# Optimization experiments

Hardware: AMD Instinct MI355X
Metric: run time of the kernel (lower is better)

Reference implementation:

```python
import jax, jax.numpy as jnp
import numpy as np

KS = 5  # kernel_size
H, W = 2048, 2048


def setup_inputs() -> dict:
    key = jax.random.key(0)
    image = jax.random.normal(key, (H, W), dtype=jnp.float32)
    return {"image": image}


def reference(image):
    ks = KS
    r = ks // 2
    h, w = image.shape
    # reflect pad (matches torch F.pad mode='reflect')
    padded = jnp.pad(image, ((r, r), (r, r)), mode="reflect")  # (h+2r, w+2r)
    # gather the ks*ks shifted views -> (h, w, ks*ks); fixed small loop over offsets
    wins = jnp.stack(
        [padded[i : i + h, j : j + w] for i in range(ks) for j in range(ks)],
        axis=-1,
    )
    # torch .median returns the lower median = sorted index (n-1)//2 (exact median here since n=25 is odd)
    srt = jnp.sort(wins, axis=-1)
    return srt[..., (ks * ks - 1) // 2]
```

## Files before the change

### kernel.cpp

```cpp
#include <hip/hip_runtime.h>

constexpr int IMG_H = 2048;
constexpr int IMG_W = 2048;
constexpr int P = 8;

#define CE(a, b) {                                              \
    float _mn, _mx;                                             \
    asm("v_min_f32 %0, %1, %2" : "=v"(_mn) : "v"(a), "v"(b));   \
    asm("v_max_f32 %0, %1, %2" : "=v"(_mx) : "v"(a), "v"(b));   \
    a = _mn; b = _mx;                                           \
}

#define SORT3(a, b, c) {                                                      \
    float _n, _d, _x;                                                         \
    asm("v_min3_f32 %0, %1, %2, %3" : "=v"(_n) : "v"(a), "v"(b), "v"(c));     \
    asm("v_med3_f32 %0, %1, %2, %3" : "=v"(_d) : "v"(a), "v"(b), "v"(c));     \
    asm("v_max3_f32 %0, %1, %2, %3" : "=v"(_x) : "v"(a), "v"(b), "v"(c));     \
    a = _n; b = _d; c = _x;                                                   \
}

__device__ __forceinline__ void sw14(float& a0, float& a1, float& a2, float& a3, float& a4,
                                     float& a5, float& a6, float& a7, float& a8, float& a9,
                                     float& a10, float& a11, float& a12, float& a13) {
    SORT3(a0, a1, a2) SORT3(a3, a4, a5) SORT3(a6, a7, a8) SORT3(a9, a10, a11) CE(a12, a13)
    SORT3(a0, a3, a6) SORT3(a0, a9, a12)
    SORT3(a2, a5, a8) SORT3(a8, a11, a13)
}
__device__ __forceinline__ void sw13(float& a0, float& a1, float& a2, float& a3, float& a4,
                                     float& a5, float& a6, float& a7, float& a8, float& a9,
                                     float& a10, float& a11, float& a12) {
    SORT3(a0, a1, a2) SORT3(a3, a4, a5) SORT3(a6, a7, a8) SORT3(a9, a10, a11)
    SORT3(a0, a3, a6) SORT3(a0, a9, a12)
    SORT3(a2, a5, a8) SORT3(a8, a11, a12)
}
__device__ __forceinline__ void sw12(float& a0, float& a1, float& a2, float& a3, float& a4,
                                     float& a5, float& a6, float& a7, float& a8, float& a9,
                                     float& a10, float& a11) {
    SORT3(a0, a1, a2) SORT3(a3, a4, a5) SORT3(a6, a7, a8) SORT3(a9, a10, a11)
    SORT3(a0, a3, a6) CE(a0, a9)
    SORT3(a2, a5, a8) CE(a8, a11)
}
__device__ __forceinline__ void sw11(float& a0, float& a1, float& a2, float& a3, float& a4,
                                     float& a5, float& a6, float& a7, float& a8, float& a9,
                                     float& a10) {
    SORT3(a0, a1, a2) SORT3(a3, a4, a5) SORT3(a6, a7, a8) CE(a9, a10)
    SORT3(a0, a3, a6) CE(a0, a9)
    SORT3(a2, a5, a8) CE(a8, a10)
}
__device__ __forceinline__ void sw10(float& a0, float& a1, float& a2, float& a3, float& a4,
                                     float& a5, float& a6, float& a7, float& a8, float& a9) {
    SORT3(a0, a1, a2) SORT3(a3, a4, a5) SORT3(a6, a7, a8)
    SORT3(a0, a3, a6) CE(a0, a9)
    SORT3(a2, a5, a8) CE(a8, a9)
}
__device__ __forceinline__ void sw9(float& a0, float& a1, float& a2, float& a3, float& a4,
                                    float& a5, float& a6, float& a7, float& a8) {
    SORT3(a0, a1, a2) SORT3(a3, a4, a5) SORT3(a6, a7, a8)
    SORT3(a0, a3, a6)
    SORT3(a2, a5, a8)
}
__device__ __forceinline__ void sw8(float& a0, float& a1, float& a2, float& a3, float& a4,
                                    float& a5, float& a6, float& a7) {
    SORT3(a0, a1, a2) SORT3(a3, a4, a5) CE(a6, a7)
    SORT3(a0, a3, a6)
    SORT3(a2, a5, a7)
}
__device__ __forceinline__ void sw7(float& a0, float& a1, float& a2, float& a3, float& a4,
                                    float& a5, float& a6) {
    SORT3(a0, a1, a2) SORT3(a3, a4, a5)
    SORT3(a0, a3, a6)
    SORT3(a2, a5, a6)
}
__device__ __forceinline__ void sw6(float& a0, float& a1, float& a2, float& a3, float& a4,
                                    float& a5) {
    SORT3(a0, a1, a2) SORT3(a3, a4, a5)
    CE(a0, a3)
    CE(a2, a5)
}

__device__ __forceinline__ float med5(float l0, float l1, float l2, float l3, float l4) {
    CE(l0, l1) CE(l2, l3)
    float a, b;
    asm("v_max_f32 %0, %1, %2" : "=v"(a) : "v"(l0), "v"(l2));
    asm("v_min_f32 %0, %1, %2" : "=v"(b) : "v"(l1), "v"(l3));
    return __builtin_amdgcn_fmed3f(a, b, l4);
}

__device__ __forceinline__ float tail5(float l1, float l2, float l3, float l4, float l5,
                                       float l6, float l7, float l8,
                                       float p0, float p1, float p2, float p3, float p4) {
    float l0 = p0;
    sw9(l0, l1, l2, l3, l4, l5, l6, l7, l8);
    l0 = p1;
    sw8(l0, l1, l2, l3, l4, l5, l6, l7);
    l0 = p2;
    sw7(l0, l1, l2, l3, l4, l5, l6);
    l0 = p3;
    sw6(l0, l1, l2, l3, l4, l5);
    l0 = p4;
    return med5(l0, l1, l2, l3, l4);
}

__device__ __forceinline__ void shared20(float s0, float s1, float s2, float s3, float s4,
                                         float s5, float s6, float s7, float s8, float s9,
                                         float s10, float s11, float s12, float s13,
                                         float s14, float s15, float s16, float s17,
                                         float s18, float s19,
                                         float& o0, float& o1, float& o2, float& o3,
                                         float& o4, float& o5, float& o6, float& o7) {
    sw14(s0, s1, s2, s3, s4, s5, s6, s7, s8, s9, s10, s11, s12, s13);
    s0 = s14;
    sw13(s0, s1, s2, s3, s4, s5, s6, s7, s8, s9, s10, s11, s12);
    s0 = s15;
    sw12(s0, s1, s2, s3, s4, s5, s6, s7, s8, s9, s10, s11);
    s0 = s16;
    sw11(s0, s1, s2, s3, s4, s5, s6, s7, s8, s9, s10);
    s0 = s17;
    sw10(s0, s1, s2, s3, s4, s5, s6, s7, s8, s9);
    s0 = s18;
    sw9(s0, s1, s2, s3, s4, s5, s6, s7, s8);
    s0 = s19;
    o0 = s0; o1 = s1; o2 = s2; o3 = s3; o4 = s4; o5 = s5; o6 = s6; o7 = s7;
}

__device__ __forceinline__ int rowbase(int r) {
    r = (r < 0) ? -r : r;
    r = (r >= IMG_H) ? 2 * IMG_H - 2 - r : r;
    return r * IMG_W;
}

#define LOADR(R, rb) {                                        \
    const int _b = (rb);                                      \
    R##0 = img[_b + c0]; R##1 = img[_b + c1];                 \
    R##2 = img[_b + c2]; R##3 = img[_b + c3];                 \
    R##4 = img[_b + c4]; R##5 = img[_b + c5];                 \
}

#define STEP(Ra, Rb, Rc, Rd, Re, Rf, yy) {                                     \
    LOADR(Rf, rowbase((yy) + 3))                                               \
    float u0, u1, u2, u3, u4, u5, u6, u7;                                      \
    shared20(Ra##1, Ra##2, Ra##3, Ra##4, Rb##1, Rb##2, Rb##3, Rb##4,           \
             Rc##1, Rc##2, Rc##3, Rc##4, Rd##1, Rd##2, Rd##3, Rd##4,           \
             Re##1, Re##2, Re##3, Re##4, u0, u1, u2, u3, u4, u5, u6, u7);      \
    const float _mL = tail5(u0, u1, u2, u3, u4, u5, u6, u7,                    \
                            Ra##0, Rb##0, Rc##0, Rd##0, Re##0);                \
    const float _mR = tail5(u0, u1, u2, u3, u4, u5, u6, u7,                    \
                            Ra##5, Rb##5, Rc##5, Rd##5, Re##5);                \
    *reinterpret_cast<float2*>(out + (yy) * IMG_W + xL) = make_float2(_mL, _mR); \
}

__global__ __launch_bounds__(256) void median5x5_strip(const float* __restrict__ img,
                                                       float* __restrict__ out) {
    const int t = blockIdx.x * blockDim.x + threadIdx.x;
    const int strip = blockIdx.y * blockDim.y + threadIdx.y;
    const int y0 = strip * P;
    const int xL = 2 * t;

    int c0 = xL - 2, c1 = xL - 1, c4 = xL + 2, c5 = xL + 3;
    c0 = (c0 < 0) ? -c0 : c0;
    c1 = (c1 < 0) ? -c1 : c1;
    c4 = (c4 >= IMG_W) ? 2 * IMG_W - 2 - c4 : c4;
    c5 = (c5 >= IMG_W) ? 2 * IMG_W - 2 - c5 : c5;
    const int c2 = xL, c3 = xL + 1;

    float A0, A1, A2, A3, A4, A5;
    float B0, B1, B2, B3, B4, B5;
    float C0, C1, C2, C3, C4, C5;
    float D0, D1, D2, D3, D4, D5;
    float E0, E1, E2, E3, E4, E5;
    float F0, F1, F2, F3, F4, F5;

    LOADR(A, rowbase(y0 - 2))
    LOADR(B, rowbase(y0 - 1))
    LOADR(C, rowbase(y0))
    LOADR(D, rowbase(y0 + 1))
    LOADR(E, rowbase(y0 + 2))

    STEP(A, B, C, D, E, F, y0 + 0)
    STEP(B, C, D, E, F, A, y0 + 1)
    STEP(C, D, E, F, A, B, y0 + 2)
    STEP(D, E, F, A, B, C, y0 + 3)
    STEP(E, F, A, B, C, D, y0 + 4)
    STEP(F, A, B, C, D, E, y0 + 5)
    STEP(A, B, C, D, E, F, y0 + 6)
    STEP(B, C, D, E, F, A, y0 + 7)
}

extern "C" void kernel_launch(void* const* d_in, const int* in_sizes, int n_in,
                              void* d_out, int out_size, void* d_ws, size_t ws_size,
                              hipStream_t stream) {
    const float* img = (const float*)d_in[0];
    float* out = (float*)d_out;
    dim3 block(64, 4);
    dim3 grid((IMG_W / 2) / 64, IMG_H / P / 4);
    median5x5_strip<<<grid, block, 0, stream>>>(img, out);
}
```

Before: 22.42 us.

## Stage 2D image tiles with halo in LDS instead of per-thread strip loads

Replaces the per-thread vertical strip kernel, which reads rows directly from global memory with a rolling register window, with a block-tiled kernel. Each block cooperatively loads a 20x132 haloed tile into shared memory with reflect-padding applied during the load, syncs, then each thread reads its 5x6 windows from LDS as float2 and computes two medians per row for 4 rows. This aims to cut redundant global loads and uncoalesced scalar reads, at the cost of a block barrier, fewer rows per thread (4 instead of 8), and LDS reads that may hit bank conflicts.

Result: slower. 24.11 us (+7.6%).

```diff
diff --git a/kernel.cpp b/kernel.cpp
--- a/kernel.cpp
+++ b/kernel.cpp
@@ -2,7 +2,10 @@
 
 constexpr int IMG_H = 2048;
 constexpr int IMG_W = 2048;
-constexpr int P = 8;
+constexpr int TW = 128;
+constexpr int TH = 16;
+constexpr int LC = TW + 4;
+constexpr int LR = TH + 4;
 
 #define CE(a, b) {                                              \
     float _mn, _mx;                                             \
@@ -123,67 +126,72 @@
     o0 = s0; o1 = s1; o2 = s2; o3 = s3; o4 = s4; o5 = s5; o6 = s6; o7 = s7;
 }
 
-__device__ __forceinline__ int rowbase(int r) {
-    r = (r < 0) ? -r : r;
-    r = (r >= IMG_H) ? 2 * IMG_H - 2 - r : r;
-    return r * IMG_W;
-}
-
-#define LOADR(R, rb) {                                        \
-    const int _b = (rb);                                      \
-    R##0 = img[_b + c0]; R##1 = img[_b + c1];                 \
-    R##2 = img[_b + c2]; R##3 = img[_b + c3];                 \
-    R##4 = img[_b + c4]; R##5 = img[_b + c5];                 \
-}
-
-#define STEP(Ra, Rb, Rc, Rd, Re, Rf, yy) {                                     \
-    LOADR(Rf, rowbase((yy) + 3))                                               \
-    float u0, u1, u2, u3, u4, u5, u6, u7;                                      \
-    shared20(Ra##1, Ra##2, Ra##3, Ra##4, Rb##1, Rb##2, Rb##3, Rb##4,           \
-             Rc##1, Rc##2, Rc##3, Rc##4, Rd##1, Rd##2, Rd##3, Rd##4,           \
-             Re##1, Re##2, Re##3, Re##4, u0, u1, u2, u3, u4, u5, u6, u7);      \
-    const float _mL = tail5(u0, u1, u2, u3, u4, u5, u6, u7,                    \
-                            Ra##0, Rb##0, Rc##0, Rd##0, Re##0);                \
-    const float _mR = tail5(u0, u1, u2, u3, u4, u5, u6, u7,                    \
-                            Ra##5, Rb##5, Rc##5, Rd##5, Re##5);                \
-    *reinterpret_cast<float2*>(out + (yy) * IMG_W + xL) = make_float2(_mL, _mR); \
-}
-
-__global__ __launch_bounds__(256) void median5x5_strip(const float* __restrict__ img,
-                                                       float* __restrict__ out) {
-    const int t = blockIdx.x * blockDim.x + threadIdx.x;
-    const int strip = blockIdx.y * blockDim.y + threadIdx.y;
-    const int y0 = strip * P;
-    const int xL = 2 * t;
-
-    int c0 = xL - 2, c1 = xL - 1, c4 = xL + 2, c5 = xL + 3;
-    c0 = (c0 < 0) ? -c0 : c0;
-    c1 = (c1 < 0) ? -c1 : c1;
-    c4 = (c4 >= IMG_W) ? 2 * IMG_W - 2 - c4 : c4;
-    c5 = (c5 >= IMG_W) ? 2 * IMG_W - 2 - c5 : c5;
-    const int c2 = xL, c3 = xL + 1;
-
-    float A0, A1, A2, A3, A4, A5;
-    float B0, B1, B2, B3, B4, B5;
-    float C0, C1, C2, C3, C4, C5;
-    float D0, D1, D2, D3, D4, D5;
-    float E0, E1, E2, E3, E4, E5;
-    float F0, F1, F2, F3, F4, F5;
-
-    LOADR(A, rowbase(y0 - 2))
-    LOADR(B, rowbase(y0 - 1))
-    LOADR(C, rowbase(y0))
-    LOADR(D, rowbase(y0 + 1))
-    LOADR(E, rowbase(y0 + 2))
-
-    STEP(A, B, C, D, E, F, y0 + 0)
-    STEP(B, C, D, E, F, A, y0 + 1)
-    STEP(C, D, E, F, A, B, y0 + 2)
-    STEP(D, E, F, A, B, C, y0 + 3)
-    STEP(E, F, A, B, C, D, y0 + 4)
-    STEP(F, A, B, C, D, E, y0 + 5)
-    STEP(A, B, C, D, E, F, y0 + 6)
-    STEP(B, C, D, E, F, A, y0 + 7)
+__global__ __launch_bounds__(256) void median5x5_tile(const float* __restrict__ img,
+                                                      float* __restrict__ out) {
+    __shared__ float lds[LR * LC];
+
+    const int tx = threadIdx.x;
+    const int ty = threadIdx.y;
+    const int x0 = blockIdx.x * TW;
+    const int y0 = blockIdx.y * TH;
+
+    const int tid = ty * 64 + tx;
+#pragma unroll
+    for (int k = 0; k < (LR * LC + 255) / 256; ++k) {
+        const int i = tid + k * 256;
+        if (i < LR * LC) {
+            const int r = i / LC;
+            const int c = i - r * LC;
+            int gr = y0 - 2 + r;
+            gr = (gr < 0) ? -gr : gr;
+            gr = (gr >= IMG_H) ? 2 * IMG_H - 2 - gr : gr;
+            int gc = x0 - 2 + c;
+            gc = (gc < 0) ? -gc : gc;
+            gc = (gc >= IMG_W) ? 2 * IMG_W - 2 - gc : gc;
+            lds[i] = img[gr * IMG_W + gc];
+        }
+    }
+    __syncthreads();
+
+    const int xL = x0 + 2 * tx;
+    const float* wbase = lds + 2 * tx;
+
+#pragma unroll
+    for (int s = 0; s < 4; ++s) {
+        const int lr = ty * 4 + s;
+        const float* p = wbase + lr * LC;
+
+        const float2 A01 = *(const float2*)(p + 0);
+        const float2 A23 = *(const float2*)(p + 2);
+        const float2 A45 = *(const float2*)(p + 4);
+        const float2 B01 = *(const float2*)(p + LC + 0);
+        const float2 B23 = *(const float2*)(p + LC + 2);
+        const float2 B45 = *(const float2*)(p + LC + 4);
+        const float2 C01 = *(const float2*)(p + 2 * LC + 0);
+        const float2 C23 = *(const float2*)(p + 2 * LC + 2);
+        const float2 C45 = *(const float2*)(p + 2 * LC + 4);
+        const float2 D01 = *(const float2*)(p + 3 * LC + 0);
+        const float2 D23 = *(const float2*)(p + 3 * LC + 2);
+        const float2 D45 = *(const float2*)(p + 3 * LC + 4);
+        const float2 E01 = *(const float2*)(p + 4 * LC + 0);
+        const float2 E23 = *(const float2*)(p + 4 * LC + 2);
+        const float2 E45 = *(const float2*)(p + 4 * LC + 4);
+
+        float u0, u1, u2, u3, u4, u5, u6, u7;
+        shared20(A01.y, A23.x, A23.y, A45.x,
+                 B01.y, B23.x, B23.y, B45.x,
+                 C01.y, C23.x, C23.y, C45.x,
+                 D01.y, D23.x, D23.y, D45.x,
+                 E01.y, E23.x, E23.y, E45.x,
+                 u0, u1, u2, u3, u4, u5, u6, u7);
+
+        const float mL = tail5(u0, u1, u2, u3, u4, u5, u6, u7,
+                               A01.x, B01.x, C01.x, D01.x, E01.x);
+        const float mR = tail5(u0, u1, u2, u3, u4, u5, u6, u7,
+                               A45.y, B45.y, C45.y, D45.y, E45.y);
+
+        *reinterpret_cast<float2*>(out + (y0 + lr) * IMG_W + xL) = make_float2(mL, mR);
+    }
 }
 
 extern "C" void kernel_launch(void* const* d_in, const int* in_sizes, int n_in,
@@ -192,6 +200,6 @@
     const float* img = (const float*)d_in[0];
     float* out = (float*)d_out;
     dim3 block(64, 4);
-    dim3 grid((IMG_W / 2) / 64, IMG_H / P / 4);
-    median5x5_strip<<<grid, block, 0, stream>>>(img, out);
-}
+    dim3 grid(IMG_W / TW, IMG_H / TH);
+    median5x5_tile<<<grid, block, 0, stream>>>(img, out);
+}
```

## Replace strip-walking horizontal pairs with one-shot vertical-pair threads

Applied to the files above, without the earlier changes.

Each thread now computes two vertically adjacent outputs in one column, sharing the sorted 4x5 middle block, instead of walking an 8-row strip for two horizontal neighbors. This removes the serial sliding-window dependence and raises thread count eightfold for more latency hiding and occupancy. In exchange each output needs roughly three times as many global loads, relying on cache hits, and the per-thread reuse across rows is lost.

Result: slower. 25.19 us (+12.3%).

```diff
diff --git a/kernel.cpp b/kernel.cpp
--- a/kernel.cpp
+++ b/kernel.cpp
@@ -2,7 +2,6 @@
 
 constexpr int IMG_H = 2048;
 constexpr int IMG_W = 2048;
-constexpr int P = 8;
 
 #define CE(a, b) {                                              \
     float _mn, _mx;                                             \
@@ -123,67 +122,52 @@
     o0 = s0; o1 = s1; o2 = s2; o3 = s3; o4 = s4; o5 = s5; o6 = s6; o7 = s7;
 }
 
-__device__ __forceinline__ int rowbase(int r) {
-    r = (r < 0) ? -r : r;
-    r = (r >= IMG_H) ? 2 * IMG_H - 2 - r : r;
-    return r * IMG_W;
-}
+__global__ __launch_bounds__(256) void median5x5_vpair(const float* __restrict__ img,
+                                                       float* __restrict__ out) {
+    const int x = blockIdx.x * 64 + threadIdx.x;
+    const int pr = blockIdx.y * 4 + threadIdx.y;
+    const int yT = 2 * pr;
 
-#define LOADR(R, rb) {                                        \
-    const int _b = (rb);                                      \
-    R##0 = img[_b + c0]; R##1 = img[_b + c1];                 \
-    R##2 = img[_b + c2]; R##3 = img[_b + c3];                 \
-    R##4 = img[_b + c4]; R##5 = img[_b + c5];                 \
-}
+    int r0 = yT - 2, r1 = yT - 1, r4 = yT + 2, r5 = yT + 3;
+    r0 = (r0 < 0) ? -r0 : r0;
+    r1 = (r1 < 0) ? -r1 : r1;
+    r4 = (r4 >= IMG_H) ? 2 * IMG_H - 2 - r4 : r4;
+    r5 = (r5 >= IMG_H) ? 2 * IMG_H - 2 - r5 : r5;
+    const int b0 = r0 * IMG_W, b1 = r1 * IMG_W, b2 = yT * IMG_W,
+              b3 = (yT + 1) * IMG_W, b4 = r4 * IMG_W, b5 = r5 * IMG_W;
 
-#define STEP(Ra, Rb, Rc, Rd, Re, Rf, yy) {                                     \
-    LOADR(Rf, rowbase((yy) + 3))                                               \
-    float u0, u1, u2, u3, u4, u5, u6, u7;                                      \
-    shared20(Ra##1, Ra##2, Ra##3, Ra##4, Rb##1, Rb##2, Rb##3, Rb##4,           \
-             Rc##1, Rc##2, Rc##3, Rc##4, Rd##1, Rd##2, Rd##3, Rd##4,           \
-             Re##1, Re##2, Re##3, Re##4, u0, u1, u2, u3, u4, u5, u6, u7);      \
-    const float _mL = tail5(u0, u1, u2, u3, u4, u5, u6, u7,                    \
-                            Ra##0, Rb##0, Rc##0, Rd##0, Re##0);                \
-    const float _mR = tail5(u0, u1, u2, u3, u4, u5, u6, u7,                    \
-                            Ra##5, Rb##5, Rc##5, Rd##5, Re##5);                \
-    *reinterpret_cast<float2*>(out + (yy) * IMG_W + xL) = make_float2(_mL, _mR); \
-}
-
-__global__ __launch_bounds__(256) void median5x5_strip(const float* __restrict__ img,
-                                                       float* __restrict__ out) {
-    const int t = blockIdx.x * blockDim.x + threadIdx.x;
-    const int strip = blockIdx.y * blockDim.y + threadIdx.y;
-    const int y0 = strip * P;
-    const int xL = 2 * t;
-
-    int c0 = xL - 2, c1 = xL - 1, c4 = xL + 2, c5 = xL + 3;
+    int c0 = x - 2, c1 = x - 1, c3 = x + 1, c4 = x + 2;
     c0 = (c0 < 0) ? -c0 : c0;
     c1 = (c1 < 0) ? -c1 : c1;
+    c3 = (c3 >= IMG_W) ? 2 * IMG_W - 2 - c3 : c3;
     c4 = (c4 >= IMG_W) ? 2 * IMG_W - 2 - c4 : c4;
-    c5 = (c5 >= IMG_W) ? 2 * IMG_W - 2 - c5 : c5;
-    const int c2 = xL, c3 = xL + 1;
+    const int c2 = x;
 
-    float A0, A1, A2, A3, A4, A5;
-    float B0, B1, B2, B3, B4, B5;
-    float C0, C1, C2, C3, C4, C5;
-    float D0, D1, D2, D3, D4, D5;
-    float E0, E1, E2, E3, E4, E5;
-    float F0, F1, F2, F3, F4, F5;
+    const float A0 = img[b0 + c0], A1 = img[b0 + c1], A2 = img[b0 + c2],
+                A3 = img[b0 + c3], A4 = img[b0 + c4];
+    const float B0 = img[b1 + c0], B1 = img[b1 + c1], B2 = img[b1 + c2],
+                B3 = img[b1 + c3], B4 = img[b1 + c4];
+    const float C0 = img[b2 + c0], C1 = img[b2 + c1], C2 = img[b2 + c2],
+                C3 = img[b2 + c3], C4 = img[b2 + c4];
+    const float D0 = img[b3 + c0], D1 = img[b3 + c1], D2 = img[b3 + c2],
+                D3 = img[b3 + c3], D4 = img[b3 + c4];
+    const float E0 = img[b4 + c0], E1 = img[b4 + c1], E2 = img[b4 + c2],
+                E3 = img[b4 + c3], E4 = img[b4 + c4];
+    const float F0 = img[b5 + c0], F1 = img[b5 + c1], F2 = img[b5 + c2],
+                F3 = img[b5 + c3], F4 = img[b5 + c4];
 
-    LOADR(A, rowbase(y0 - 2))
-    LOADR(B, rowbase(y0 - 1))
-    LOADR(C, rowbase(y0))
-    LOADR(D, rowbase(y0 + 1))
-    LOADR(E, rowbase(y0 + 2))
+    float u0, u1, u2, u3, u4, u5, u6, u7;
+    shared20(B0, B1, B2, B3, B4,
+             C0, C1, C2, C3, C4,
+             D0, D1, D2, D3, D4,
+             E0, E1, E2, E3, E4,
+             u0, u1, u2, u3, u4, u5, u6, u7);
 
-    STEP(A, B, C, D, E, F, y0 + 0)
-    STEP(B, C, D, E, F, A, y0 + 1)
-    STEP(C, D, E, F, A, B, y0 + 2)
-    STEP(D, E, F, A, B, C, y0 + 3)
-    STEP(E, F, A, B, C, D, y0 + 4)
-    STEP(F, A, B, C, D, E, y0 + 5)
-    STEP(A, B, C, D, E, F, y0 + 6)
-    STEP(B, C, D, E, F, A, y0 + 7)
+    const float mT = tail5(u0, u1, u2, u3, u4, u5, u6, u7, A0, A1, A2, A3, A4);
+    const float mB = tail5(u0, u1, u2, u3, u4, u5, u6, u7, F0, F1, F2, F3, F4);
+
+    out[b2 + x] = mT;
+    out[b3 + x] = mB;
 }
 
 extern "C" void kernel_launch(void* const* d_in, const int* in_sizes, int n_in,
@@ -192,6 +176,6 @@
     const float* img = (const float*)d_in[0];
     float* out = (float*)d_out;
     dim3 block(64, 4);
-    dim3 grid((IMG_W / 2) / 64, IMG_H / P / 4);
-    median5x5_strip<<<grid, block, 0, stream>>>(img, out);
+    dim3 grid(IMG_W / 64, (IMG_H / 2) / 4);
+    median5x5_vpair<<<grid, block, 0, stream>>>(img, out);
 }
```
